# Optimization experiments

Hardware: AMD Instinct MI355X
Metric: run time of the kernel (lower is better)

Reference implementation:

```python
import jax, jax.numpy as jnp
import numpy as np

LOG2 = float(np.log(2.0))

def _mlp(x, W, b):
    # SchNet-style MLP block: Linear + shifted softplus activation
    return jax.nn.softplus(x @ W + b) - LOG2

def setup_inputs() -> dict:
    key = jax.random.key(0)
    ks = jax.random.split(key, 9)
    E, N, R, F, O = 1_600_000, 50_000, 64, 64, 64
    s = 1.0 / np.sqrt(F)
    return {
        "bf": jax.random.normal(ks[0], (E, R), dtype=jnp.float32),
        "eh": jax.random.normal(ks[1], (E, F), dtype=jnp.float32),
        "W1": jax.random.normal(ks[2], (R, F), dtype=jnp.float32) * s,
        "b1": jax.random.normal(ks[3], (F,), dtype=jnp.float32) * s,
        "W2": jax.random.normal(ks[4], (F, F), dtype=jnp.float32) * s,
        "b2": jax.random.normal(ks[5], (F,), dtype=jnp.float32) * s,
        "W3": jax.random.normal(ks[6], (F, O), dtype=jnp.float32) * s,
        "b3": jax.random.normal(ks[7], (O,), dtype=jnp.float32) * s,
        "dst": jax.random.randint(ks[8], (E,), 0, N, dtype=jnp.int32),
        "num_nodes": N,
    }

def reference(bf, eh, W1, b1, W2, b2, W3, b3, dst, num_nodes):
    # Edge filter-generating network: two MLPs on radial basis features
    w = _mlp(_mlp(bf, W1, b1), W2, b2)          # [E, F]
    m = w * eh                                   # gated edge messages [E, F]
    # scatter-mean onto destination nodes (dgl copy_e + mean)
    sums = jax.ops.segment_sum(m, dst, num_segments=num_nodes)              # [N, F]
    cnt = jax.ops.segment_sum(jnp.ones((m.shape[0],), m.dtype), dst,
                              num_segments=num_nodes)                        # [N]
    h = sums / jnp.maximum(cnt, 1.0)[:, None]    # mean; 0 for isolated nodes
    return _mlp(h, W3, b3)                       # interaction-block MLP [N, O]
```

## Files before the change

### kernel.cpp

```cpp
#include <hip/hip_runtime.h>
#include <hip/hip_bf16.h>

#define LOG2F_ 0.69314718055994530942f

typedef __attribute__((ext_vector_type(8))) short s8bf;
typedef __attribute__((ext_vector_type(4))) float f32x4;
typedef __attribute__((ext_vector_type(4))) unsigned u32x4;

__device__ __forceinline__ float ssp(float x) {
    float e = __expf(-fabsf(x));
    return __logf(1.0f + e) + fmaxf(x, 0.0f) - LOG2F_;
}
__device__ __forceinline__ short bf_hi(float x) {
    __hip_bfloat16 h = __float2bfloat16(x);
    return *reinterpret_cast<short*>(&h);
}
__device__ __forceinline__ float bf_to_f(short s) {
    __hip_bfloat16 h;
    *reinterpret_cast<short*>(&h) = s;
    return __bfloat162float(h);
}
__device__ __forceinline__ unsigned pkhi(float a, float b) {
    return (__float_as_uint(a) >> 16) | (__float_as_uint(b) & 0xFFFF0000u);
}
__device__ __forceinline__ unsigned pklo(float a, float b) {
    float ra = a - __uint_as_float(__float_as_uint(a) & 0xFFFF0000u);
    float rb = b - __uint_as_float(__float_as_uint(b) & 0xFFFF0000u);
    return (__float_as_uint(ra) >> 16) | (__float_as_uint(rb) & 0xFFFF0000u);
}

__global__ __launch_bounds__(256) void hist_kernel(const int* __restrict__ dst,
                                                   int* __restrict__ hist,
                                                   int* __restrict__ rnk, int E) {
    const int i0 = (blockIdx.x * blockDim.x + threadIdx.x) * 4;
    if (i0 + 3 < E) {
        int4 d = *(const int4*)(dst + i0);
        int4 r;
        r.x = atomicAdd(&hist[d.x], 1);
        r.y = atomicAdd(&hist[d.y], 1);
        r.z = atomicAdd(&hist[d.z], 1);
        r.w = atomicAdd(&hist[d.w], 1);
        *(int4*)(rnk + i0) = r;
    } else {
        for (int j = 0; j < 4; ++j)
            if (i0 + j < E) rnk[i0 + j] = atomicAdd(&hist[dst[i0 + j]], 1);
    }
}

__global__ __launch_bounds__(256) void scan_part(const int* __restrict__ h,
                                                 int* __restrict__ bsum, int N) {
    const int i0 = blockIdx.x * 1024 + threadIdx.x * 4;
    int s = 0;
    #pragma unroll
    for (int j = 0; j < 4; ++j) { int i = i0 + j; if (i < N) s += h[i]; }
    __shared__ int red[4];
    const int lane = threadIdx.x & 63, w = threadIdx.x >> 6;
    #pragma unroll
    for (int off = 32; off; off >>= 1) s += __shfl_down(s, off, 64);
    if (lane == 0) red[w] = s;
    __syncthreads();
    if (threadIdx.x == 0) bsum[blockIdx.x] = red[0] + red[1] + red[2] + red[3];
}

__global__ void scan_top(int* __restrict__ bsum, int nb) {
    const int lane = threadIdx.x;
    if (nb <= 64) {
        int v = (lane < nb) ? bsum[lane] : 0;
        int inc = v;
        #pragma unroll
        for (int off = 1; off < 64; off <<= 1) {
            int o = __shfl_up(inc, off, 64);
            if (lane >= off) inc += o;
        }
        if (lane < nb) bsum[lane] = inc - v;
    } else if (lane == 0) {
        int run = 0;
        for (int i = 0; i < nb; ++i) { int t = bsum[i]; bsum[i] = run; run += t; }
    }
}

__global__ __launch_bounds__(256) void scan_local(const int* __restrict__ h,
                                                  const int* __restrict__ bsum,
                                                  int* __restrict__ cursor, int N) {
    const int i0 = blockIdx.x * 1024 + threadIdx.x * 4;
    int v[4]; int s = 0;
    #pragma unroll
    for (int j = 0; j < 4; ++j) { int i = i0 + j; v[j] = (i < N) ? h[i] : 0; s += v[j]; }
    const int lane = threadIdx.x & 63, w = threadIdx.x >> 6;
    int inc = s;
    #pragma unroll
    for (int off = 1; off < 64; off <<= 1) {
        int o = __shfl_up(inc, off, 64);
        if (lane >= off) inc += o;
    }
    __shared__ int wsum[4];
    if (lane == 63) wsum[w] = inc;
    __syncthreads();
    int run = bsum[blockIdx.x];
    for (int i = 0; i < w; ++i) run += wsum[i];
    run += inc - s;
    #pragma unroll
    for (int j = 0; j < 4; ++j) { int i = i0 + j; if (i < N) cursor[i] = run; run += v[j]; }
}

__global__ __launch_bounds__(256) void meta_kernel(const int* __restrict__ dst,
                                                   const int* __restrict__ cursor,
                                                   const int* __restrict__ rnk,
                                                   int2* __restrict__ meta, int E) {
    const int i0 = (blockIdx.x * blockDim.x + threadIdx.x) * 4;
    if (i0 + 3 < E) {
        int4 d = *(const int4*)(dst + i0);
        int4 r = *(const int4*)(rnk + i0);
        meta[cursor[d.x] + r.x] = make_int2(i0,     d.x);
        meta[cursor[d.y] + r.y] = make_int2(i0 + 1, d.y);
        meta[cursor[d.z] + r.z] = make_int2(i0 + 2, d.z);
        meta[cursor[d.w] + r.w] = make_int2(i0 + 3, d.w);
    } else {
        for (int j = 0; j < 4; ++j)
            if (i0 + j < E) {
                int dd = dst[i0 + j];
                meta[cursor[dd] + rnk[i0 + j]] = make_int2(i0 + j, dd);
            }
    }
}

#define WFRAG(woff, nt, k0i) \
    (*(const s8bf*)(lds + (woff) + ((((nt) << 1) + (k0i)) << 10) + (lane << 4)))

__global__ __launch_bounds__(256, 3) void edge_kernel(
    const float* __restrict__ bf, const float* __restrict__ eh,
    const float* __restrict__ W1, const float* __restrict__ b1,
    const float* __restrict__ W2, const float* __restrict__ b2,
    const int2* __restrict__ meta,
    float* __restrict__ sums, int E)
{
    __shared__ __align__(16) unsigned char lds[49152];

    const int tid  = threadIdx.x;
    const int lane = tid & 63;
    const int wv   = tid >> 6;
    const int g    = lane >> 4;
    const int n16  = lane & 15;

    {
        float* wst = (float*)(lds + 32768);
        for (int i = tid; i < 4096; i += 256) wst[i] = W1[i];
        __syncthreads();
        for (int u = tid; u < 512; u += 256) {
            const int f = u >> 6, nt = f >> 1, k0i = f & 1;
            const int gg = (u >> 4) & 3, nn = u & 15;
            s8bf hi, lo;
            #pragma unroll
            for (int j = 0; j < 8; ++j) {
                float v = wst[(k0i * 32 + gg * 8 + j) * 64 + nt * 16 + nn];
                short h = bf_hi(v);
                hi[j] = h; lo[j] = bf_hi(v - bf_to_f(h));
            }
            *(s8bf*)(lds + (u << 4)) = hi;
            *(s8bf*)(lds + 8192 + (u << 4)) = lo;
        }
        __syncthreads();
        for (int i = tid; i < 4096; i += 256) wst[i] = W2[i];
        __syncthreads();
        for (int u = tid; u < 512; u += 256) {
            const int f = u >> 6, nt = f >> 1, k0i = f & 1;
            const int gg = (u >> 4) & 3, nn = u & 15;
            s8bf hi, lo;
            #pragma unroll
            for (int j = 0; j < 8; ++j) {
                float v = wst[(k0i * 32 + gg * 8 + j) * 64 + nt * 16 + nn];
                short h = bf_hi(v);
                hi[j] = h; lo[j] = bf_hi(v - bf_to_f(h));
            }
            *(s8bf*)(lds + 16384 + (u << 4)) = hi;
            *(s8bf*)(lds + 24576 + (u << 4)) = lo;
        }
        __syncthreads();
    }

    float b1v[4], b2v[4];
    #pragma unroll
    for (int nt = 0; nt < 4; ++nt) { b1v[nt] = b1[nt*16 + n16]; b2v[nt] = b2[nt*16 + n16]; }

    unsigned char* wb = lds + 32768 + (wv << 12);
    char* Xh = (char*)wb;
    char* Xl = (char*)wb + 2048;

    const int r4   = lane >> 2;
    const int c16  = (lane & 3) << 4;
    const int s0   = (lane & 3) << 1;
    const int crow = g << 2;
    const int sw_n = (n16 & 7) << 4;

    const int wave_id = (blockIdx.x << 2) + wv;
    const int nwaves  = gridDim.x << 2;
    const int ntiles  = (E + 15) >> 4;
    const int lastE   = E - 1;

    int eiv0 = 0, eiv1 = 0, dsv0 = 0, dsv1 = 0;
    float xs[16];
    {
        const int t1 = wave_id + nwaves;
        if (lane < 16) {
            if (wave_id < ntiles) {
                const int2 mv = meta[min(wave_id * 16 + lane, lastE)];
                eiv0 = mv.x; dsv0 = mv.y;
            }
            if (t1 < ntiles) {
                const int2 mv = meta[min(t1 * 16 + lane, lastE)];
                eiv1 = mv.x; dsv1 = mv.y;
            }
        }
        if (wave_id < ntiles) {
            const int ri = __shfl(eiv0, r4, 64);
            const size_t roff = (size_t)(unsigned)ri * 64 + c16;
            *(float4*)&xs[0]  = *(const float4*)(bf + roff);
            *(float4*)&xs[4]  = *(const float4*)(bf + roff + 4);
            *(float4*)&xs[8]  = *(const float4*)(bf + roff + 8);
            *(float4*)&xs[12] = *(const float4*)(bf + roff + 12);
        }
    }

    for (int t = wave_id; t < ntiles; t += nwaves) {
        const int base = t << 4;

        u32x4 hv0, hv1, lv0, lv1;
        #pragma unroll
        for (int j = 0; j < 4; ++j) {
            hv0[j] = pkhi(xs[2*j],     xs[2*j + 1]);
            lv0[j] = pklo(xs[2*j],     xs[2*j + 1]);
            hv1[j] = pkhi(xs[8 + 2*j], xs[8 + 2*j + 1]);
            lv1[j] = pklo(xs[8 + 2*j], xs[8 + 2*j + 1]);
        }
        {
            const int sw = (r4 & 7) << 4;
            const int a0 = r4 * 128 + ((s0 << 4) ^ sw);
            const int a1 = r4 * 128 + (((s0 + 1) << 4) ^ sw);
            *(u32x4*)(Xh + a0) = hv0;  *(u32x4*)(Xh + a1) = hv1;
            *(u32x4*)(Xl + a0) = lv0;  *(u32x4*)(Xl + a1) = lv1;
        }

        float evs[16];
        #pragma unroll
        for (int e = 0; e < 16; ++e) {
            const int ei = __builtin_amdgcn_readlane(eiv0, e);
            evs[e] = eh[(size_t)(unsigned)ei * 64 + lane];
        }

        const int tn1 = t + nwaves, tn2 = t + 2 * nwaves;
        if (tn1 < ntiles) {
            const int ri = __shfl(eiv1, r4, 64);
            const size_t roff = (size_t)(unsigned)ri * 64 + c16;
            *(float4*)&xs[0]  = *(const float4*)(bf + roff);
            *(float4*)&xs[4]  = *(const float4*)(bf + roff + 4);
            *(float4*)&xs[8]  = *(const float4*)(bf + roff + 8);
            *(float4*)&xs[12] = *(const float4*)(bf + roff + 12);
        }

        int eiv_n = 0, dsv_n = 0;
        if (lane < 16 && tn2 < ntiles) {
            const int2 mv = meta[min(tn2 * 16 + lane, lastE)];
            eiv_n = mv.x; dsv_n = mv.y;
        }

        f32x4 acc[4];
        #pragma unroll
        for (int nt = 0; nt < 4; ++nt) acc[nt] = (f32x4){0.f, 0.f, 0.f, 0.f};
        #pragma unroll
        for (int k0i = 0; k0i < 2; ++k0i) {
            const int ab = (n16 << 7) + (((((k0i << 2) + g)) << 4) ^ sw_n);
            s8bf ah = *(s8bf*)(Xh + ab);
            s8bf al = *(s8bf*)(Xl + ab);
            s8bf wh0 = WFRAG(0, 0, k0i), wh1 = WFRAG(0, 1, k0i),
                 wh2 = WFRAG(0, 2, k0i), wh3 = WFRAG(0, 3, k0i);
            s8bf wl0 = WFRAG(8192, 0, k0i), wl1 = WFRAG(8192, 1, k0i),
                 wl2 = WFRAG(8192, 2, k0i), wl3 = WFRAG(8192, 3, k0i);
            __builtin_amdgcn_s_setprio(1);
            acc[0] = __builtin_amdgcn_mfma_f32_16x16x32_bf16(ah, wh0, acc[0], 0, 0, 0);
            acc[0] = __builtin_amdgcn_mfma_f32_16x16x32_bf16(ah, wl0, acc[0], 0, 0, 0);
            acc[0] = __builtin_amdgcn_mfma_f32_16x16x32_bf16(al, wh0, acc[0], 0, 0, 0);
            acc[1] = __builtin_amdgcn_mfma_f32_16x16x32_bf16(ah, wh1, acc[1], 0, 0, 0);
            acc[1] = __builtin_amdgcn_mfma_f32_16x16x32_bf16(ah, wl1, acc[1], 0, 0, 0);
            acc[1] = __builtin_amdgcn_mfma_f32_16x16x32_bf16(al, wh1, acc[1], 0, 0, 0);
            acc[2] = __builtin_amdgcn_mfma_f32_16x16x32_bf16(ah, wh2, acc[2], 0, 0, 0);
            acc[2] = __builtin_amdgcn_mfma_f32_16x16x32_bf16(ah, wl2, acc[2], 0, 0, 0);
            acc[2] = __builtin_amdgcn_mfma_f32_16x16x32_bf16(al, wh2, acc[2], 0, 0, 0);
            acc[3] = __builtin_amdgcn_mfma_f32_16x16x32_bf16(ah, wh3, acc[3], 0, 0, 0);
            acc[3] = __builtin_amdgcn_mfma_f32_16x16x32_bf16(ah, wl3, acc[3], 0, 0, 0);
            acc[3] = __builtin_amdgcn_mfma_f32_16x16x32_bf16(al, wh3, acc[3], 0, 0, 0);
            __builtin_amdgcn_s_setprio(0);
        }

        #pragma unroll
        for (int nt = 0; nt < 4; ++nt)
            #pragma unroll
            for (int r = 0; r < 4; ++r) {
                const int row = crow + r;
                *(float*)(wb + (row << 8) +
                          ((((nt * 16 + n16) << 2)) ^ ((row & 7) << 4))) =
                    ssp(acc[nt][r] + b1v[nt]);
            }

        f32x4 acc2[4];
        #pragma unroll
        for (int nt = 0; nt < 4; ++nt) acc2[nt] = (f32x4){0.f, 0.f, 0.f, 0.f};
        #pragma unroll
        for (int k0i = 0; k0i < 2; ++k0i) {
            const int bc = (k0i << 7) + (g << 5);
            const int rb = n16 << 8;
            f32x4 f0 = *(f32x4*)(wb + rb + (bc ^ sw_n));
            f32x4 f1 = *(f32x4*)(wb + rb + ((bc + 16) ^ sw_n));
            u32x4 ahu, alu;
            ahu[0] = pkhi(f0[0], f0[1]); ahu[1] = pkhi(f0[2], f0[3]);
            ahu[2] = pkhi(f1[0], f1[1]); ahu[3] = pkhi(f1[2], f1[3]);
            alu[0] = pklo(f0[0], f0[1]); alu[1] = pklo(f0[2], f0[3]);
            alu[2] = pklo(f1[0], f1[1]); alu[3] = pklo(f1[2], f1[3]);
            s8bf ah = *(s8bf*)&ahu;
            s8bf al = *(s8bf*)&alu;
            s8bf wh0 = WFRAG(16384, 0, k0i), wh1 = WFRAG(16384, 1, k0i),
                 wh2 = WFRAG(16384, 2, k0i), wh3 = WFRAG(16384, 3, k0i);
            s8bf wl0 = WFRAG(24576, 0, k0i), wl1 = WFRAG(24576, 1, k0i),
                 wl2 = WFRAG(24576, 2, k0i), wl3 = WFRAG(24576, 3, k0i);
            __builtin_amdgcn_s_setprio(1);
            acc2[0] = __builtin_amdgcn_mfma_f32_16x16x32_bf16(ah, wh0, acc2[0], 0, 0, 0);
            acc2[0] = __builtin_amdgcn_mfma_f32_16x16x32_bf16(ah, wl0, acc2[0], 0, 0, 0);
            acc2[0] = __builtin_amdgcn_mfma_f32_16x16x32_bf16(al, wh0, acc2[0], 0, 0, 0);
            acc2[1] = __builtin_amdgcn_mfma_f32_16x16x32_bf16(ah, wh1, acc2[1], 0, 0, 0);
            acc2[1] = __builtin_amdgcn_mfma_f32_16x16x32_bf16(ah, wl1, acc2[1], 0, 0, 0);
            acc2[1] = __builtin_amdgcn_mfma_f32_16x16x32_bf16(al, wh1, acc2[1], 0, 0, 0);
            acc2[2] = __builtin_amdgcn_mfma_f32_16x16x32_bf16(ah, wh2, acc2[2], 0, 0, 0);
            acc2[2] = __builtin_amdgcn_mfma_f32_16x16x32_bf16(ah, wl2, acc2[2], 0, 0, 0);
            acc2[2] = __builtin_amdgcn_mfma_f32_16x16x32_bf16(al, wh2, acc2[2], 0, 0, 0);
            acc2[3] = __builtin_amdgcn_mfma_f32_16x16x32_bf16(ah, wh3, acc2[3], 0, 0, 0);
            acc2[3] = __builtin_amdgcn_mfma_f32_16x16x32_bf16(ah, wl3, acc2[3], 0, 0, 0);
            acc2[3] = __builtin_amdgcn_mfma_f32_16x16x32_bf16(al, wh3, acc2[3], 0, 0, 0);
            __builtin_amdgcn_s_setprio(0);
        }

        #pragma unroll
        for (int nt = 0; nt < 4; ++nt)
            #pragma unroll
            for (int r = 0; r < 4; ++r) {
                const int row = crow + r;
                *(float*)(wb + (row << 8) +
                          ((((nt * 16 + n16) << 2)) ^ ((row & 7) << 4))) =
                    ssp(acc2[nt][r] + b2v[nt]);
            }

        {
            float accv = 0.f;
            int cur = -1;
            #pragma unroll
            for (int e = 0; e < 16; ++e) {
                if (base + e < E) {
                    const int d = __builtin_amdgcn_readlane(dsv0, e);
                    const float mv = *(const float*)(wb + (e << 8) +
                                        ((lane << 2) ^ ((e & 7) << 4))) * evs[e];
                    if (d != cur) {
                        if (cur >= 0) atomicAdd(&sums[(size_t)cur * 64 + lane], accv);
                        accv = mv; cur = d;
                    } else {
                        accv += mv;
                    }
                }
            }
            if (cur >= 0) atomicAdd(&sums[(size_t)cur * 64 + lane], accv);
        }

        eiv0 = eiv1; eiv1 = eiv_n;
        dsv0 = dsv1; dsv1 = dsv_n;
    }
}

__global__ __launch_bounds__(256) void node_kernel(
    const float* __restrict__ sums, const int* __restrict__ hist,
    const float* __restrict__ W3, const float* __restrict__ b3,
    float* __restrict__ out, int N)
{
    __shared__ float sW[64][64];
    __shared__ float sb[64];
    __shared__ float sC[64];
    __shared__ float sX[64][65];

    const int tid = threadIdx.x;
    for (int i = tid; i < 4096; i += 256) sW[i >> 6][i & 63] = W3[i];
    if (tid < 64) sb[tid] = b3[tid];

    const int f4 = (tid & 15) << 2;
    const int e4 = (tid >> 4) << 2;
    const int ntiles = (N + 63) >> 6;

    for (int t = blockIdx.x; t < ntiles; t += gridDim.x) {
        const int base = t << 6;
        __syncthreads();
        if (tid < 64) {
            int gn = base + tid;
            sC[tid] = (gn < N) ? 1.0f / fmaxf((float)hist[gn], 1.0f) : 0.0f;
        }
        __syncthreads();
        #pragma unroll
        for (int k = 0; k < 16; ++k) {
            int idx = (k << 8) + tid;
            int n = idx >> 6, r = idx & 63;
            int gn = base + n;
            sX[n][r] = (gn < N) ? sums[(size_t)gn * 64 + r] * sC[n] : 0.0f;
        }
        __syncthreads();

        float acc[4][4] = {{0.f,0.f,0.f,0.f},{0.f,0.f,0.f,0.f},
                           {0.f,0.f,0.f,0.f},{0.f,0.f,0.f,0.f}};
        #pragma unroll 8
        for (int r = 0; r < 64; ++r) {
            float xv[4];
            #pragma unroll
            for (int i = 0; i < 4; ++i) xv[i] = sX[e4 + i][r];
            float4 w4 = *(const float4*)&sW[r][f4];
            #pragma unroll
            for (int i = 0; i < 4; ++i) {
                acc[i][0] = fmaf(xv[i], w4.x, acc[i][0]);
                acc[i][1] = fmaf(xv[i], w4.y, acc[i][1]);
                acc[i][2] = fmaf(xv[i], w4.z, acc[i][2]);
                acc[i][3] = fmaf(xv[i], w4.w, acc[i][3]);
            }
        }

        #pragma unroll
        for (int i = 0; i < 4; ++i) {
            int gn = base + e4 + i;
            if (gn < N) {
                float4 o;
                o.x = ssp(acc[i][0] + sb[f4 + 0]);
                o.y = ssp(acc[i][1] + sb[f4 + 1]);
                o.z = ssp(acc[i][2] + sb[f4 + 2]);
                o.w = ssp(acc[i][3] + sb[f4 + 3]);
                *(float4*)&out[(size_t)gn * 64 + f4] = o;
            }
        }
    }
}

extern "C" void kernel_launch(void* const* d_in, const int* in_sizes, int n_in,
                              void* d_out, int out_size, void* d_ws, size_t ws_size,
                              hipStream_t stream) {
    const float* bf = (const float*)d_in[0];
    const float* eh = (const float*)d_in[1];
    const float* W1 = (const float*)d_in[2];
    const float* b1 = (const float*)d_in[3];
    const float* W2 = (const float*)d_in[4];
    const float* b2 = (const float*)d_in[5];
    const float* W3 = (const float*)d_in[6];
    const float* b3 = (const float*)d_in[7];
    const int*   dst = (const int*)d_in[8];

    const int E = in_sizes[0] / 64;
    const int N = out_size / 64;

    float* sums    = (float*)d_ws;
    int*   hist    = (int*)(sums + (size_t)N * 64);
    int*   cursor  = hist + N;
    int*   rnk     = cursor + N;
    int2*  meta    = (int2*)(rnk + E);
    int*   bsum    = (int*)(meta + E);

    hipMemsetAsync(d_ws, 0, (size_t)N * 64 * sizeof(float) + N * sizeof(int), stream);

    const int gE4 = (E + 1023) / 1024;
    const int nb  = (N + 1023) >> 10;
    hist_kernel<<<gE4, 256, 0, stream>>>(dst, hist, rnk, E);
    scan_part<<<nb, 256, 0, stream>>>(hist, bsum, N);
    scan_top<<<1, 64, 0, stream>>>(bsum, nb);
    scan_local<<<nb, 256, 0, stream>>>(hist, bsum, cursor, N);
    meta_kernel<<<gE4, 256, 0, stream>>>(dst, cursor, rnk, meta, E);

    edge_kernel<<<768, 256, 0, stream>>>(bf, eh, W1, b1, W2, b2, meta, sums, E);

    const int ntilesN = (N + 63) >> 6;
    node_kernel<<<ntilesN, 256, 0, stream>>>(sums, hist, W3, b3, (float*)d_out, N);
}
```

Baseline: 374.5 us.

## Process 32-edge tiles per wave to reuse weight fragments across two M-tiles

Doubles the per-wave edge tile from 16 to 32 rows so each weight fragment loaded from LDS feeds two MFMA row blocks. The per-wave scratch buffer doubles, LDS grows to 64KB, and occupancy drops from 3 to 2 blocks per CU with a smaller grid. This cuts LDS weight reads per edge and loop overhead per edge, at the cost of more registers, fewer resident waves to hide the gather latency, and longer atomic-reduction runs.

Measured after the change: 388.8 us. 1.04x slower.

```diff
diff --git a/kernel.cpp b/kernel.cpp
--- a/kernel.cpp
+++ b/kernel.cpp
@@ -127,14 +127,14 @@
 #define WFRAG(woff, nt, k0i) \
     (*(const s8bf*)(lds + (woff) + ((((nt) << 1) + (k0i)) << 10) + (lane << 4)))
 
-__global__ __launch_bounds__(256, 3) void edge_kernel(
+__global__ __launch_bounds__(256, 2) void edge_kernel(
     const float* __restrict__ bf, const float* __restrict__ eh,
     const float* __restrict__ W1, const float* __restrict__ b1,
     const float* __restrict__ W2, const float* __restrict__ b2,
     const int2* __restrict__ meta,
     float* __restrict__ sums, int E)
 {
-    __shared__ __align__(16) unsigned char lds[49152];
+    __shared__ __align__(16) unsigned char lds[65536];
 
     const int tid  = threadIdx.x;
     const int lane = tid & 63;
@@ -182,176 +182,177 @@
     #pragma unroll
     for (int nt = 0; nt < 4; ++nt) { b1v[nt] = b1[nt*16 + n16]; b2v[nt] = b2[nt*16 + n16]; }
 
-    unsigned char* wb = lds + 32768 + (wv << 12);
+    unsigned char* wb = lds + 32768 + (wv << 13);
     char* Xh = (char*)wb;
-    char* Xl = (char*)wb + 2048;
-
-    const int r4   = lane >> 2;
-    const int c16  = (lane & 3) << 4;
-    const int s0   = (lane & 3) << 1;
+    char* Xl = (char*)wb + 4096;
+
+    const int r2   = lane >> 1;
+    const int ch   = lane & 1;
     const int crow = g << 2;
     const int sw_n = (n16 & 7) << 4;
 
     const int wave_id = (blockIdx.x << 2) + wv;
     const int nwaves  = gridDim.x << 2;
-    const int ntiles  = (E + 15) >> 4;
+    const int ntiles  = (E + 31) >> 5;
     const int lastE   = E - 1;
 
     int eiv0 = 0, eiv1 = 0, dsv0 = 0, dsv1 = 0;
-    float xs[16];
+    float xs[32];
     {
         const int t1 = wave_id + nwaves;
-        if (lane < 16) {
+        if (lane < 32) {
             if (wave_id < ntiles) {
-                const int2 mv = meta[min(wave_id * 16 + lane, lastE)];
+                const int2 mv = meta[min(wave_id * 32 + lane, lastE)];
                 eiv0 = mv.x; dsv0 = mv.y;
             }
             if (t1 < ntiles) {
-                const int2 mv = meta[min(t1 * 16 + lane, lastE)];
+                const int2 mv = meta[min(t1 * 32 + lane, lastE)];
                 eiv1 = mv.x; dsv1 = mv.y;
             }
         }
         if (wave_id < ntiles) {
-            const int ri = __shfl(eiv0, r4, 64);
-            const size_t roff = (size_t)(unsigned)ri * 64 + c16;
-            *(float4*)&xs[0]  = *(const float4*)(bf + roff);
-            *(float4*)&xs[4]  = *(const float4*)(bf + roff + 4);
-            *(float4*)&xs[8]  = *(const float4*)(bf + roff + 8);
-            *(float4*)&xs[12] = *(const float4*)(bf + roff + 12);
+            const int ri = __shfl(eiv0, r2, 64);
+            const size_t roff = (size_t)(unsigned)ri * 64 + (ch << 5);
+            #pragma unroll
+            for (int q = 0; q < 8; ++q)
+                *(float4*)&xs[q * 4] = *(const float4*)(bf + roff + q * 4);
         }
     }
 
     for (int t = wave_id; t < ntiles; t += nwaves) {
-        const int base = t << 4;
-
-        u32x4 hv0, hv1, lv0, lv1;
-        #pragma unroll
-        for (int j = 0; j < 4; ++j) {
-            hv0[j] = pkhi(xs[2*j],     xs[2*j + 1]);
-            lv0[j] = pklo(xs[2*j],     xs[2*j + 1]);
-            hv1[j] = pkhi(xs[8 + 2*j], xs[8 + 2*j + 1]);
-            lv1[j] = pklo(xs[8 + 2*j], xs[8 + 2*j + 1]);
-        }
+        const int base = t << 5;
+
         {
-            const int sw = (r4 & 7) << 4;
-            const int a0 = r4 * 128 + ((s0 << 4) ^ sw);
-            const int a1 = r4 * 128 + (((s0 + 1) << 4) ^ sw);
-            *(u32x4*)(Xh + a0) = hv0;  *(u32x4*)(Xh + a1) = hv1;
-            *(u32x4*)(Xl + a0) = lv0;  *(u32x4*)(Xl + a1) = lv1;
-        }
-
-        float evs[16];
-        #pragma unroll
-        for (int e = 0; e < 16; ++e) {
+            const int sw = (r2 & 7) << 4;
+            #pragma unroll
+            for (int s = 0; s < 4; ++s) {
+                u32x4 hv, lv;
+                #pragma unroll
+                for (int j = 0; j < 4; ++j) {
+                    hv[j] = pkhi(xs[8*s + 2*j], xs[8*s + 2*j + 1]);
+                    lv[j] = pklo(xs[8*s + 2*j], xs[8*s + 2*j + 1]);
+                }
+                const int a = r2 * 128 + ((((ch << 2) + s) << 4) ^ sw);
+                *(u32x4*)(Xh + a) = hv;
+                *(u32x4*)(Xl + a) = lv;
+            }
+        }
+
+        float evs[32];
+        #pragma unroll
+        for (int e = 0; e < 32; ++e) {
             const int ei = __builtin_amdgcn_readlane(eiv0, e);
             evs[e] = eh[(size_t)(unsigned)ei * 64 + lane];
         }
 
         const int tn1 = t + nwaves, tn2 = t + 2 * nwaves;
         if (tn1 < ntiles) {
-            const int ri = __shfl(eiv1, r4, 64);
-            const size_t roff = (size_t)(unsigned)ri * 64 + c16;
-            *(float4*)&xs[0]  = *(const float4*)(bf + roff);
-            *(float4*)&xs[4]  = *(const float4*)(bf + roff + 4);
-            *(float4*)&xs[8]  = *(const float4*)(bf + roff + 8);
-            *(float4*)&xs[12] = *(const float4*)(bf + roff + 12);
+            const int ri = __shfl(eiv1, r2, 64);
+            const size_t roff = (size_t)(unsigned)ri * 64 + (ch << 5);
+            #pragma unroll
+            for (int q = 0; q < 8; ++q)
+                *(float4*)&xs[q * 4] = *(const float4*)(bf + roff + q * 4);
         }
 
         int eiv_n = 0, dsv_n = 0;
-        if (lane < 16 && tn2 < ntiles) {
-            const int2 mv = meta[min(tn2 * 16 + lane, lastE)];
+        if (lane < 32 && tn2 < ntiles) {
+            const int2 mv = meta[min(tn2 * 32 + lane, lastE)];
             eiv_n = mv.x; dsv_n = mv.y;
         }
 
-        f32x4 acc[4];
-        #pragma unroll
-        for (int nt = 0; nt < 4; ++nt) acc[nt] = (f32x4){0.f, 0.f, 0.f, 0.f};
+        f32x4 acc[2][4];
+        #pragma unroll
+        for (int m = 0; m < 2; ++m)
+            #pragma unroll
+            for (int nt = 0; nt < 4; ++nt) acc[m][nt] = (f32x4){0.f, 0.f, 0.f, 0.f};
         #pragma unroll
         for (int k0i = 0; k0i < 2; ++k0i) {
-            const int ab = (n16 << 7) + (((((k0i << 2) + g)) << 4) ^ sw_n);
-            s8bf ah = *(s8bf*)(Xh + ab);
-            s8bf al = *(s8bf*)(Xl + ab);
-            s8bf wh0 = WFRAG(0, 0, k0i), wh1 = WFRAG(0, 1, k0i),
-                 wh2 = WFRAG(0, 2, k0i), wh3 = WFRAG(0, 3, k0i);
-            s8bf wl0 = WFRAG(8192, 0, k0i), wl1 = WFRAG(8192, 1, k0i),
-                 wl2 = WFRAG(8192, 2, k0i), wl3 = WFRAG(8192, 3, k0i);
+            const int so = (((k0i << 2) + g) << 4) ^ sw_n;
+            s8bf ah0 = *(s8bf*)(Xh + (n16 << 7) + so);
+            s8bf al0 = *(s8bf*)(Xl + (n16 << 7) + so);
+            s8bf ah1 = *(s8bf*)(Xh + ((16 + n16) << 7) + so);
+            s8bf al1 = *(s8bf*)(Xl + ((16 + n16) << 7) + so);
             __builtin_amdgcn_s_setprio(1);
-            acc[0] = __builtin_amdgcn_mfma_f32_16x16x32_bf16(ah, wh0, acc[0], 0, 0, 0);
-            acc[0] = __builtin_amdgcn_mfma_f32_16x16x32_bf16(ah, wl0, acc[0], 0, 0, 0);
-            acc[0] = __builtin_amdgcn_mfma_f32_16x16x32_bf16(al, wh0, acc[0], 0, 0, 0);
-            acc[1] = __builtin_amdgcn_mfma_f32_16x16x32_bf16(ah, wh1, acc[1], 0, 0, 0);
-            acc[1] = __builtin_amdgcn_mfma_f32_16x16x32_bf16(ah, wl1, acc[1], 0, 0, 0);
-            acc[1] = __builtin_amdgcn_mfma_f32_16x16x32_bf16(al, wh1, acc[1], 0, 0, 0);
-            acc[2] = __builtin_amdgcn_mfma_f32_16x16x32_bf16(ah, wh2, acc[2], 0, 0, 0);
-            acc[2] = __builtin_amdgcn_mfma_f32_16x16x32_bf16(ah, wl2, acc[2], 0, 0, 0);
-            acc[2] = __builtin_amdgcn_mfma_f32_16x16x32_bf16(al, wh2, acc[2], 0, 0, 0);
-            acc[3] = __builtin_amdgcn_mfma_f32_16x16x32_bf16(ah, wh3, acc[3], 0, 0, 0);
-            acc[3] = __builtin_amdgcn_mfma_f32_16x16x32_bf16(ah, wl3, acc[3], 0, 0, 0);
-            acc[3] = __builtin_amdgcn_mfma_f32_16x16x32_bf16(al, wh3, acc[3], 0, 0, 0);
+            #pragma unroll
+            for (int nt = 0; nt < 4; ++nt) {
+                s8bf wh = WFRAG(0, nt, k0i);
+                s8bf wl = WFRAG(8192, nt, k0i);
+                acc[0][nt] = __builtin_amdgcn_mfma_f32_16x16x32_bf16(ah0, wh, acc[0][nt], 0, 0, 0);
+                acc[0][nt] = __builtin_amdgcn_mfma_f32_16x16x32_bf16(ah0, wl, acc[0][nt], 0, 0, 0);
+                acc[0][nt] = __builtin_amdgcn_mfma_f32_16x16x32_bf16(al0, wh, acc[0][nt], 0, 0, 0);
+                acc[1][nt] = __builtin_amdgcn_mfma_f32_16x16x32_bf16(ah1, wh, acc[1][nt], 0, 0, 0);
+                acc[1][nt] = __builtin_amdgcn_mfma_f32_16x16x32_bf16(ah1, wl, acc[1][nt], 0, 0, 0);
+                acc[1][nt] = __builtin_amdgcn_mfma_f32_16x16x32_bf16(al1, wh, acc[1][nt], 0, 0, 0);
+            }
             __builtin_amdgcn_s_setprio(0);
         }
 
         #pragma unroll
-        for (int nt = 0; nt < 4; ++nt)
-            #pragma unroll
-            for (int r = 0; r < 4; ++r) {
-                const int row = crow + r;
-                *(float*)(wb + (row << 8) +
-                          ((((nt * 16 + n16) << 2)) ^ ((row & 7) << 4))) =
-                    ssp(acc[nt][r] + b1v[nt]);
-            }
-
-        f32x4 acc2[4];
-        #pragma unroll
-        for (int nt = 0; nt < 4; ++nt) acc2[nt] = (f32x4){0.f, 0.f, 0.f, 0.f};
+        for (int m = 0; m < 2; ++m)
+            #pragma unroll
+            for (int nt = 0; nt < 4; ++nt)
+                #pragma unroll
+                for (int r = 0; r < 4; ++r) {
+                    const int row = m * 16 + crow + r;
+                    *(float*)(wb + (row << 8) +
+                              ((((nt * 16 + n16) << 2)) ^ ((row & 7) << 4))) =
+                        ssp(acc[m][nt][r] + b1v[nt]);
+                }
+
+        f32x4 acc2[2][4];
+        #pragma unroll
+        for (int m = 0; m < 2; ++m)
+            #pragma unroll
+            for (int nt = 0; nt < 4; ++nt) acc2[m][nt] = (f32x4){0.f, 0.f, 0.f, 0.f};
         #pragma unroll
         for (int k0i = 0; k0i < 2; ++k0i) {
             const int bc = (k0i << 7) + (g << 5);
-            const int rb = n16 << 8;
-            f32x4 f0 = *(f32x4*)(wb + rb + (bc ^ sw_n));
-            f32x4 f1 = *(f32x4*)(wb + rb + ((bc + 16) ^ sw_n));
-            u32x4 ahu, alu;
-            ahu[0] = pkhi(f0[0], f0[1]); ahu[1] = pkhi(f0[2], f0[3]);
-            ahu[2] = pkhi(f1[0], f1[1]); ahu[3] = pkhi(f1[2], f1[3]);
-            alu[0] = pklo(f0[0], f0[1]); alu[1] = pklo(f0[2], f0[3]);
-            alu[2] = pklo(f1[0], f1[1]); alu[3] = pklo(f1[2], f1[3]);
-            s8bf ah = *(s8bf*)&ahu;
-            s8bf al = *(s8bf*)&alu;
-            s8bf wh0 = WFRAG(16384, 0, k0i), wh1 = WFRAG(16384, 1, k0i),
-                 wh2 = WFRAG(16384, 2, k0i), wh3 = WFRAG(16384, 3, k0i);
-            s8bf wl0 = WFRAG(24576, 0, k0i), wl1 = WFRAG(24576, 1, k0i),
-                 wl2 = WFRAG(24576, 2, k0i), wl3 = WFRAG(24576, 3, k0i);
+            s8bf ahm[2], alm[2];
+            #pragma unroll
+            for (int m = 0; m < 2; ++m) {
+                const int rb = (m * 16 + n16) << 8;
+                f32x4 f0 = *(f32x4*)(wb + rb + (bc ^ sw_n));
+                f32x4 f1 = *(f32x4*)(wb + rb + ((bc + 16) ^ sw_n));
+                u32x4 ahu, alu;
+                ahu[0] = pkhi(f0[0], f0[1]); ahu[1] = pkhi(f0[2], f0[3]);
+                ahu[2] = pkhi(f1[0], f1[1]); ahu[3] = pkhi(f1[2], f1[3]);
+                alu[0] = pklo(f0[0], f0[1]); alu[1] = pklo(f0[2], f0[3]);
+                alu[2] = pklo(f1[0], f1[1]); alu[3] = pklo(f1[2], f1[3]);
+                ahm[m] = *(s8bf*)&ahu;
+                alm[m] = *(s8bf*)&alu;
+            }
             __builtin_amdgcn_s_setprio(1);
-            acc2[0] = __builtin_amdgcn_mfma_f32_16x16x32_bf16(ah, wh0, acc2[0], 0, 0, 0);
-            acc2[0] = __builtin_amdgcn_mfma_f32_16x16x32_bf16(ah, wl0, acc2[0], 0, 0, 0);
-            acc2[0] = __builtin_amdgcn_mfma_f32_16x16x32_bf16(al, wh0, acc2[0], 0, 0, 0);
-            acc2[1] = __builtin_amdgcn_mfma_f32_16x16x32_bf16(ah, wh1, acc2[1], 0, 0, 0);
-            acc2[1] = __builtin_amdgcn_mfma_f32_16x16x32_bf16(ah, wl1, acc2[1], 0, 0, 0);
-            acc2[1] = __builtin_amdgcn_mfma_f32_16x16x32_bf16(al, wh1, acc2[1], 0, 0, 0);
-            acc2[2] = __builtin_amdgcn_mfma_f32_16x16x32_bf16(ah, wh2, acc2[2], 0, 0, 0);
-            acc2[2] = __builtin_amdgcn_mfma_f32_16x16x32_bf16(ah, wl2, acc2[2], 0, 0, 0);
-            acc2[2] = __builtin_amdgcn_mfma_f32_16x16x32_bf16(al, wh2, acc2[2], 0, 0, 0);
-            acc2[3] = __builtin_amdgcn_mfma_f32_16x16x32_bf16(ah, wh3, acc2[3], 0, 0, 0);
-            acc2[3] = __builtin_amdgcn_mfma_f32_16x16x32_bf16(ah, wl3, acc2[3], 0, 0, 0);
-            acc2[3] = __builtin_amdgcn_mfma_f32_16x16x32_bf16(al, wh3, acc2[3], 0, 0, 0);
+            #pragma unroll
+            for (int nt = 0; nt < 4; ++nt) {
+                s8bf wh = WFRAG(16384, nt, k0i);
+                s8bf wl = WFRAG(24576, nt, k0i);
+                acc2[0][nt] = __builtin_amdgcn_mfma_f32_16x16x32_bf16(ahm[0], wh, acc2[0][nt], 0, 0, 0);
+                acc2[0][nt] = __builtin_amdgcn_mfma_f32_16x16x32_bf16(ahm[0], wl, acc2[0][nt], 0, 0, 0);
+                acc2[0][nt] = __builtin_amdgcn_mfma_f32_16x16x32_bf16(alm[0], wh, acc2[0][nt], 0, 0, 0);
+                acc2[1][nt] = __builtin_amdgcn_mfma_f32_16x16x32_bf16(ahm[1], wh, acc2[1][nt], 0, 0, 0);
+                acc2[1][nt] = __builtin_amdgcn_mfma_f32_16x16x32_bf16(ahm[1], wl, acc2[1][nt], 0, 0, 0);
+                acc2[1][nt] = __builtin_amdgcn_mfma_f32_16x16x32_bf16(alm[1], wh, acc2[1][nt], 0, 0, 0);
+            }
             __builtin_amdgcn_s_setprio(0);
         }
 
         #pragma unroll
-        for (int nt = 0; nt < 4; ++nt)
-            #pragma unroll
-            for (int r = 0; r < 4; ++r) {
-                const int row = crow + r;
-                *(float*)(wb + (row << 8) +
-                          ((((nt * 16 + n16) << 2)) ^ ((row & 7) << 4))) =
-                    ssp(acc2[nt][r] + b2v[nt]);
-            }
+        for (int m = 0; m < 2; ++m)
+            #pragma unroll
+            for (int nt = 0; nt < 4; ++nt)
+                #pragma unroll
+                for (int r = 0; r < 4; ++r) {
+                    const int row = m * 16 + crow + r;
+                    *(float*)(wb + (row << 8) +
+                              ((((nt * 16 + n16) << 2)) ^ ((row & 7) << 4))) =
+                        ssp(acc2[m][nt][r] + b2v[nt]);
+                }
 
         {
             float accv = 0.f;
             int cur = -1;
             #pragma unroll
-            for (int e = 0; e < 16; ++e) {
+            for (int e = 0; e < 32; ++e) {
                 if (base + e < E) {
                     const int d = __builtin_amdgcn_readlane(dsv0, e);
                     const float mv = *(const float*)(wb + (e << 8) +
@@ -472,7 +473,7 @@
     scan_local<<<nb, 256, 0, stream>>>(hist, bsum, cursor, N);
     meta_kernel<<<gE4, 256, 0, stream>>>(dst, cursor, rnk, meta, E);
 
-    edge_kernel<<<768, 256, 0, stream>>>(bf, eh, W1, b1, W2, b2, meta, sums, E);
+    edge_kernel<<<512, 256, 0, stream>>>(bf, eh, W1, b1, W2, b2, meta, sums, E);
 
     const int ntilesN = (N + 63) >> 6;
     node_kernel<<<ntilesN, 256, 0, stream>>>(sums, hist, W3, b3, (float*)d_out, N);
```
